# Optimization experiments

Hardware: AMD Instinct MI355X
Metric: run time of the kernel (lower is better)

Reference implementation:

```python
import jax, jax.numpy as jnp
import numpy as np

# MolFormer TestBert config (from checkpoint hyper_parameters)
B, T, D, H, L, F, V = 64, 250, 768, 12, 12, 32, 2362
DH = D // H  # head dim = 64
EPS = 1e-6   # fast_transformers LinearAttention eps


def _layernorm(x, g, b):
    m = x.mean(-1, keepdims=True)
    v = ((x - m) ** 2).mean(-1, keepdims=True)
    return (x - m) / jnp.sqrt(v + 1e-5) * g + b


def setup_inputs() -> dict:
    key = jax.random.key(0)
    ks = jax.random.split(key, 20)
    s = 0.02

    def n(k, shape, scale=s):
        return jax.random.normal(k, shape, dtype=jnp.float32) * scale

    mask = jax.random.randint(ks[1], (B, T), 0, 2).astype(bool)
    mask = mask.at[:, 0].set(True)  # keep CLS position valid
    return {
        "batch": jax.random.randint(ks[0], (B, T), 0, V),
        "mask": mask,
        "tok_emb": n(ks[2], (V, D)),
        "pos_emb": n(ks[3], (1, T, D)),
        "Wq": n(ks[4], (L, D, D)), "bq": jnp.zeros((L, D)),
        "Wk": n(ks[5], (L, D, D)), "bk": jnp.zeros((L, D)),
        "Wv": n(ks[6], (L, D, D)), "bv": jnp.zeros((L, D)),
        "Wo": n(ks[7], (L, D, D)), "bo": jnp.zeros((L, D)),
        # GeneralizedRandomFeatures random projection omega: [L, head_dim, n_feats]
        "omega": jax.random.normal(ks[8], (L, DH, F), dtype=jnp.float32),
        "ln1_g": jnp.ones((L, D)), "ln1_b": jnp.zeros((L, D)),
        "ln2_g": jnp.ones((L, D)), "ln2_b": jnp.zeros((L, D)),
        # feed_forward_dimensions == n_embd in the builder kwargs
        "W1": n(ks[9], (L, D, D)), "b1": jnp.zeros((L, D)),
        "W2": n(ks[10], (L, D, D)), "b2": jnp.zeros((L, D)),
    }


def reference(batch, mask, tok_emb, pos_emb, Wq, bq, Wk, bk, Wv, bv, Wo, bo,
              omega, ln1_g, ln1_b, ln2_g, ln2_b, W1, b1, W2, b2):
    Bc, Tc = batch.shape
    # LengthMask(mask.sum(-1)) -> prefix key mask
    lengths = mask.astype(jnp.int32).sum(-1)
    key_mask = (jnp.arange(Tc)[None, :] < lengths[:, None]).astype(jnp.float32)  # [B,T]

    x = tok_emb[batch] + pos_emb[:, :Tc, :]  # dropout = identity in eval
    attn_w = None
    for l in range(L):
        q = (x @ Wq[l] + bq[l]).reshape(Bc, Tc, H, DH)
        k = (x @ Wk[l] + bk[l]).reshape(Bc, Tc, H, DH)
        v = (x @ Wv[l] + bv[l]).reshape(Bc, Tc, H, DH)
        # GeneralizedRandomFeatures: phi(x) = relu(x @ omega)
        Qf = jax.nn.relu(jnp.einsum('bthd,df->bthf', q, omega[l]))
        Kf = jax.nn.relu(jnp.einsum('bshd,df->bshf', k, omega[l]))
        Kf = Kf * key_mask[:, :, None, None]
        # linear attention: out = phi(Q) (phi(K)^T V) / (phi(Q) . sum phi(K))
        KV = jnp.einsum('bshf,bshm->bhfm', Kf, v)
        Z = 1.0 / (jnp.einsum('bthf,bhf->bth', Qf, Kf.sum(axis=1)) + EPS)
        out = jnp.einsum('bthf,bhfm,bth->bthm', Qf, KV, Z)
        if l == L - 1:
            # 'linearwweights': the implied (normalized) attention matrix
            attn_w = jnp.einsum('bthf,bshf,bth->bhts', Qf, Kf, Z)
        out = out.reshape(Bc, Tc, D) @ Wo[l] + bo[l]
        # fast_transformers post-norm encoder layer
        x = _layernorm(x + out, ln1_g[l], ln1_b[l])
        y = jax.nn.gelu(x @ W1[l] + b1[l], approximate=False) @ W2[l] + b2[l]
        x = _layernorm(x + y, ln2_g[l], ln2_b[l])
    # mode == 'cls'
    return x[:, 0, :], attn_w
```

## Files before the change

kernel.cpp:

```cpp
#include <hip/hip_runtime.h>
#include <hip/hip_bf16.h>

typedef __hip_bfloat16 bf16;
typedef __attribute__((ext_vector_type(4))) float f32x4;
typedef __attribute__((ext_vector_type(8))) short bf16x8;
typedef __attribute__((ext_vector_type(4))) short short4v;

#define B_ 64
#define T_ 250
#define D_ 768
#define H_ 12
#define DH_ 64
#define F_ 32
#define L_ 12
#define BT_ (B_*T_)
#define NF_ (H_*F_)
#define QKVN_ (3*D_)
#define KVTN_ 80

static __device__ __forceinline__ float b2f(short s) {
    union { float f; unsigned u; } z; z.u = ((unsigned)(unsigned short)s) << 16; return z.f;
}
static __device__ __forceinline__ short f2bs(float f) {
    bf16 b = __float2bfloat16(f);
    return *(short*)&b;
}

__global__ void lengths_kernel(const unsigned char* __restrict__ mask, int* __restrict__ lengths) {
    __shared__ int not_i32, not_f32;
    const unsigned int* w = (const unsigned int*)mask;
    int tid = threadIdx.x;
    if (tid == 0) { not_i32 = 0; not_f32 = 0; }
    __syncthreads();
    int li = 0, lf = 0;
    for (int i = tid; i < 4000; i += 256) {
        unsigned int v = w[i];
        if (v > 1u) li = 1;
        if (v != 0u && v != 0x3F800000u) lf = 1;
    }
    if (li) not_i32 = 1;
    if (lf) not_f32 = 1;
    __syncthreads();
    int mode = (!not_i32) ? 0 : ((!not_f32) ? 1 : 2);
    if (tid < B_) {
        int cnt = 0;
        if (mode == 0) {
            const int* r = (const int*)mask + tid * T_;
            for (int t = 0; t < T_; ++t) cnt += (r[t] != 0);
        } else if (mode == 1) {
            const unsigned int* r = w + tid * T_;
            for (int t = 0; t < T_; ++t) cnt += (r[t] != 0);
        } else {
            const unsigned char* r = mask + tid * T_;
            for (int t = 0; t < T_; ++t) cnt += (r[t] != 0);
        }
        lengths[tid] = cnt;
    }
}

__global__ void embed_kernel(const int* __restrict__ batch, const float* __restrict__ tok,
                             const float* __restrict__ pos, float* __restrict__ x,
                             bf16* __restrict__ xb) {
    int bt = blockIdx.x;
    int t = bt % T_;
    int tok_id = batch[bt];
    const float* tr = tok + (size_t)tok_id * D_;
    const float* pr = pos + (size_t)t * D_;
    float* xr = x + (size_t)bt * D_;
    bf16* xbr = xb + (size_t)bt * D_;
    for (int d = threadIdx.x; d < D_; d += 256) {
        float v = tr[d] + pr[d];
        xr[d] = v;
        xbr[d] = __float2bfloat16(v);
    }
}

__global__ __launch_bounds__(256) void transpose_w_all(
    const float* __restrict__ Wq, const float* __restrict__ Wk, const float* __restrict__ Wv,
    const float* __restrict__ Wo, const float* __restrict__ W1, const float* __restrict__ W2,
    bf16* __restrict__ Wt)
{
    __shared__ float tile[32][33];
    int zz = blockIdx.z;
    int l = zz / 6, m = zz - l * 6;
    const float* src;
    switch (m) {
        case 0: src = Wq; break; case 1: src = Wk; break; case 2: src = Wv; break;
        case 3: src = Wo; break; case 4: src = W1; break; default: src = W2; break;
    }
    src += (size_t)l * D_ * D_;
    bf16* dst = Wt + (size_t)zz * D_ * D_;
    int k0 = blockIdx.y * 32, n0 = blockIdx.x * 32;
    int tx = threadIdx.x, ty = threadIdx.y;
#pragma unroll
    for (int i = 0; i < 4; ++i)
        tile[ty + i * 8][tx] = src[(size_t)(k0 + ty + i * 8) * D_ + n0 + tx];
    __syncthreads();
#pragma unroll
    for (int i = 0; i < 4; ++i)
        dst[(size_t)(n0 + ty + i * 8) * D_ + k0 + tx] = __float2bfloat16(tile[tx][ty + i * 8]);
}

__global__ void pack_bias(const float* __restrict__ bq, const float* __restrict__ bk,
                          const float* __restrict__ bv, float* __restrict__ qkvb) {
    int o = blockIdx.x * 256 + threadIdx.x;
    if (o >= L_ * QKVN_) return;
    int l = o / QKVN_, c = o - l * QKVN_;
    float v;
    if (c < D_) v = bq[l * D_ + c];
    else if (c < 2 * D_) v = bk[l * D_ + c - D_];
    else v = bv[l * D_ + c - 2 * D_];
    qkvb[o] = v;
}

#define GP_SLOT 20480
__global__ __launch_bounds__(512, 2) void gemm_pipe(
    const bf16* __restrict__ A, const bf16* __restrict__ Bt,
    const float* __restrict__ bias, bf16* __restrict__ C,
    int N, int lda, int ldc, int act, const int* __restrict__ lengths)
{
    __shared__ __attribute__((aligned(16))) short lds_s[3 * GP_SLOT];
    const int tid = threadIdx.x, lane = tid & 63, wave = tid >> 6;
    const int wm = wave >> 2, wn = wave & 3;
    const int rsel = lane & 15, kq = lane >> 4;

    const int gx = gridDim.x;
    const int nwg = gx * gridDim.y;
    int orig = blockIdx.y * gx + blockIdx.x;
    int q = nwg >> 3, r = nwg & 7;
    int xcd = orig & 7, idx = orig >> 3;
    int swz = (xcd < r) ? xcd * (q + 1) + idx : r * (q + 1) + (xcd - r) * q + idx;
    const int row0 = (swz / gx) * 128;
    const int col0 = (swz % gx) * 192;

    const short* gA[2];
    const short* gB[3];
#pragma unroll
    for (int i = 0; i < 2; ++i) {
        int seg = (i * 8 + wave) * 64 + lane;
        int rr = seg >> 3, kb = (seg & 7) ^ (rr & 7);
        gA[i] = (const short*)A + (size_t)(row0 + rr) * lda + kb * 8;
    }
#pragma unroll
    for (int i = 0; i < 3; ++i) {
        int seg = (i * 8 + wave) * 64 + lane;
        int rr = seg >> 3, kb = (seg & 7) ^ (rr & 7);
        gB[i] = (const short*)Bt + (size_t)(col0 + rr) * 768 + kb * 8;
    }

    f32x4 acc[4][3];
#pragma unroll
    for (int i = 0; i < 4; ++i)
#pragma unroll
        for (int j = 0; j < 3; ++j) acc[i][j] = (f32x4){0.f, 0.f, 0.f, 0.f};

    auto STAGE = [&](int kt, int slot) {
        short* base = lds_s + slot * GP_SLOT;
        int kcol = kt * 64;
#pragma unroll
        for (int i = 0; i < 2; ++i) {
            int segb = (i * 8 + wave) * 64;
            __builtin_amdgcn_global_load_lds(
                (const __attribute__((address_space(1))) unsigned int*)(gA[i] + kcol),
                (__attribute__((address_space(3))) unsigned int*)(base + segb * 8), 16, 0, 0);
        }
#pragma unroll
        for (int i = 0; i < 3; ++i) {
            int segb = (i * 8 + wave) * 64;
            __builtin_amdgcn_global_load_lds(
                (const __attribute__((address_space(1))) unsigned int*)(gB[i] + kcol),
                (__attribute__((address_space(3))) unsigned int*)(base + 8192 + segb * 8), 16, 0, 0);
        }
    };

    auto COMPUTE = [&](int slot) {
        const short* sA = lds_s + slot * GP_SLOT;
        const short* sB = sA + 8192;
        bf16x8 bfv[3][2];
#pragma unroll
        for (int n = 0; n < 3; ++n)
#pragma unroll
            for (int ks = 0; ks < 2; ++ks) {
                int rr = wn * 48 + n * 16 + rsel;
                int kb = ks * 4 + kq;
                bfv[n][ks] = *(const bf16x8*)(sB + rr * 64 + ((kb ^ (rr & 7)) << 3));
            }
#pragma unroll
        for (int mp = 0; mp < 2; ++mp) {
            bf16x8 af[2][2];
#pragma unroll
            for (int mi = 0; mi < 2; ++mi)
#pragma unroll
                for (int ks = 0; ks < 2; ++ks) {
                    int rr = wm * 64 + (mp * 2 + mi) * 16 + rsel;
                    int kb = ks * 4 + kq;
                    af[mi][ks] = *(const bf16x8*)(sA + rr * 64 + ((kb ^ (rr & 7)) << 3));
                }
            __builtin_amdgcn_s_setprio(1);
#pragma unroll
            for (int mi = 0; mi < 2; ++mi)
#pragma unroll
                for (int n = 0; n < 3; ++n)
#pragma unroll
                    for (int ks = 0; ks < 2; ++ks)
                        acc[mp * 2 + mi][n] = __builtin_amdgcn_mfma_f32_16x16x32_bf16(
                            af[mi][ks], bfv[n][ks], acc[mp * 2 + mi][n], 0, 0, 0);
            __builtin_amdgcn_s_setprio(0);
        }
    };

    STAGE(0, 0); STAGE(1, 1); STAGE(2, 2);
    asm volatile("s_waitcnt vmcnt(10)" ::: "memory");
    __builtin_amdgcn_s_barrier();

    int slot = 0;
    for (int kt = 0; kt < 12; ++kt) {
        COMPUTE(slot);
        if (kt < 11) {
            __builtin_amdgcn_s_barrier();
            if (kt <= 8) {
                STAGE(kt + 3, slot);
                asm volatile("s_waitcnt vmcnt(10)" ::: "memory");
            } else if (kt == 9) {
                asm volatile("s_waitcnt vmcnt(5)" ::: "memory");
            } else {
                asm volatile("s_waitcnt vmcnt(0)" ::: "memory");
            }
            __builtin_amdgcn_s_barrier();
        }
        slot = (slot == 2) ? 0 : slot + 1;
    }

    float bj[3];
#pragma unroll
    for (int n = 0; n < 3; ++n) {
        int col = col0 + wn * 48 + n * 16 + rsel;
        bj[n] = bias ? bias[col] : 0.f;
    }
#pragma unroll
    for (int m = 0; m < 4; ++m) {
#pragma unroll
        for (int rr = 0; rr < 4; ++rr) {
            int row = row0 + wm * 64 + m * 16 + (kq << 2) + rr;
            bool kill = false;
            if (act == 3) { int b = row / T_; int t = row - b * T_; kill = (t >= lengths[b]); }
            size_t base = (size_t)row * ldc + col0 + wn * 48 + rsel;
#pragma unroll
            for (int n = 0; n < 3; ++n) {
                float v = acc[m][n][rr] + bj[n];
                if (act == 1) v = 0.5f * v * (1.0f + erff(v * 0.70710678118654752f));
                else if (act >= 2) v = fmaxf(v, 0.f);
                if (kill) v = 0.f;
                C[base + n * 16] = __float2bfloat16(v);
            }
        }
    }
}

__global__ __launch_bounds__(256) void feat_kernel(
    const bf16* __restrict__ qkv, const float* __restrict__ om,
    bf16* __restrict__ Qf, bf16* __restrict__ Kf, const int* __restrict__ lengths)
{
    __shared__ __attribute__((aligned(16))) short omT[32 * 64];
    int z = blockIdx.z, h = blockIdx.y;
    int row0 = blockIdx.x * 128;
    int tid = threadIdx.x, lane = tid & 63, wave = tid >> 6;
    {
        int f = tid >> 3, k0 = (tid & 7) * 8;
#pragma unroll
        for (int j = 0; j < 8; ++j)
            omT[f * 64 + k0 + j] = f2bs(om[(size_t)(k0 + j) * F_ + f]);
    }
    __syncthreads();

    const short* A = (const short*)qkv + (size_t)z * D_ + h * DH_;
    int rsel = lane & 15, kof = (lane >> 4) << 3;

    bf16x8 af[2][2], bfr[2][2];
#pragma unroll
    for (int mi = 0; mi < 2; ++mi) {
        int row = row0 + wave * 32 + mi * 16 + rsel;
#pragma unroll
        for (int ks = 0; ks < 2; ++ks)
            af[mi][ks] = *(const bf16x8*)(A + (size_t)row * QKVN_ + ks * 32 + kof);
    }
#pragma unroll
    for (int ni = 0; ni < 2; ++ni)
#pragma unroll
        for (int ks = 0; ks < 2; ++ks)
            bfr[ni][ks] = *(const bf16x8*)(omT + (ni * 16 + rsel) * 64 + ks * 32 + kof);

    f32x4 acc[2][2];
#pragma unroll
    for (int i = 0; i < 2; ++i)
#pragma unroll
        for (int j = 0; j < 2; ++j) acc[i][j] = (f32x4){0.f, 0.f, 0.f, 0.f};
#pragma unroll
    for (int mi = 0; mi < 2; ++mi)
#pragma unroll
        for (int ni = 0; ni < 2; ++ni)
#pragma unroll
            for (int ks = 0; ks < 2; ++ks)
                acc[mi][ni] = __builtin_amdgcn_mfma_f32_16x16x32_bf16(af[mi][ks], bfr[ni][ks], acc[mi][ni], 0, 0, 0);

    bf16* out = z ? Kf : Qf;
#pragma unroll
    for (int mi = 0; mi < 2; ++mi) {
#pragma unroll
        for (int r = 0; r < 4; ++r) {
            int row = row0 + wave * 32 + mi * 16 + ((lane >> 4) << 2) + r;
            bool kill = false;
            if (z) { int b = row / T_; int t = row - b * T_; kill = (t >= lengths[b]); }
#pragma unroll
            for (int ni = 0; ni < 2; ++ni) {
                float v = fmaxf(acc[mi][ni][r], 0.f);
                if (kill) v = 0.f;
                out[(size_t)row * NF_ + h * F_ + ni * 16 + rsel] = __float2bfloat16(v);
            }
        }
    }
}

__global__ __launch_bounds__(256) void kvsum_kernel(
    const bf16* __restrict__ Kf, const bf16* __restrict__ v, int ldv,
    bf16* __restrict__ KVt)
{
    __shared__ short KfS[64][36];
    __shared__ short vS[64][68];
    int h = blockIdx.x, b = blockIdx.y;
    int tid = threadIdx.x, lane = tid & 63, wv = tid >> 6;
    int lr = tid >> 2, cp = tid & 3;

    const short* Kg = (const short*)Kf + (size_t)(b * T_) * NF_ + h * F_;
    const short* Vg = (const short*)v + (size_t)(b * T_) * ldv + h * DH_;

    f32x4 acc[2];
    acc[0] = (f32x4){0.f, 0.f, 0.f, 0.f};
    acc[1] = (f32x4){0.f, 0.f, 0.f, 0.f};
    float ksacc = 0.f;

    for (int s0 = 0; s0 < T_; s0 += 64) {
        __syncthreads();
        int s = s0 + lr;
        if (s < T_) {
            bf16x8 k8 = *(const bf16x8*)(Kg + (size_t)s * NF_ + cp * 8);
            *(short4v*)&KfS[lr][cp * 8]     = *((const short4v*)&k8);
            *(short4v*)&KfS[lr][cp * 8 + 4] = *((const short4v*)&k8 + 1);
            bf16x8 v8a = *(const bf16x8*)(Vg + (size_t)s * ldv + cp * 16);
            bf16x8 v8b = *(const bf16x8*)(Vg + (size_t)s * ldv + cp * 16 + 8);
            *(short4v*)&vS[lr][cp * 16]      = *((const short4v*)&v8a);
            *(short4v*)&vS[lr][cp * 16 + 4]  = *((const short4v*)&v8a + 1);
            *(short4v*)&vS[lr][cp * 16 + 8]  = *((const short4v*)&v8b);
            *(short4v*)&vS[lr][cp * 16 + 12] = *((const short4v*)&v8b + 1);
        } else {
            short4v zz = (short4v){0, 0, 0, 0};
            *(short4v*)&KfS[lr][cp * 8]     = zz;
            *(short4v*)&KfS[lr][cp * 8 + 4] = zz;
            *(short4v*)&vS[lr][cp * 16]      = zz;
            *(short4v*)&vS[lr][cp * 16 + 4]  = zz;
            *(short4v*)&vS[lr][cp * 16 + 8]  = zz;
            *(short4v*)&vS[lr][cp * 16 + 12] = zz;
        }
        __syncthreads();
        if (tid < 32) {
            float p0 = 0.f, p1 = 0.f;
            for (int ss = 0; ss < 64; ss += 2) {
                p0 += b2f(KfS[ss][tid]);
                p1 += b2f(KfS[ss + 1][tid]);
            }
            ksacc += p0 + p1;
        }
        bf16x8 af0[2], af1[2], bfr[2];
#pragma unroll
        for (int ks = 0; ks < 2; ++ks) {
            int sb = ks * 32 + ((lane >> 4) << 3);
#pragma unroll
            for (int j = 0; j < 8; ++j) {
                ((short*)&af0[ks])[j] = KfS[sb + j][lane & 15];
                ((short*)&af1[ks])[j] = KfS[sb + j][16 + (lane & 15)];
                ((short*)&bfr[ks])[j] = vS[sb + j][wv * 16 + (lane & 15)];
            }
        }
#pragma unroll
        for (int ks = 0; ks < 2; ++ks) {
            acc[0] = __builtin_amdgcn_mfma_f32_16x16x32_bf16(af0[ks], bfr[ks], acc[0], 0, 0, 0);
            acc[1] = __builtin_amdgcn_mfma_f32_16x16x32_bf16(af1[ks], bfr[ks], acc[1], 0, 0, 0);
        }
    }

    bf16* dst = KVt + (size_t)(b * H_ + h) * KVTN_ * F_;
    int m = wv * 16 + (lane & 15);
#pragma unroll
    for (int mi = 0; mi < 2; ++mi) {
#pragma unroll
        for (int r = 0; r < 4; ++r) {
            int f = mi * 16 + ((lane >> 4) << 2) + r;
            dst[(size_t)m * F_ + f] = __float2bfloat16(acc[mi][r]);
        }
    }
    if (tid < 32) dst[(size_t)64 * F_ + tid] = __float2bfloat16(ksacc);
    if (tid < 240) {
        ((short*)dst)[65 * F_ + tid * 2]     = 0;
        ((short*)dst)[65 * F_ + tid * 2 + 1] = 0;
    }
}

__global__ __launch_bounds__(256) void attn_mfma(
    const bf16* __restrict__ Qf, const bf16* __restrict__ KVt,
    float* __restrict__ Z, bf16* __restrict__ out, int ldo)
{
    int h = blockIdx.x, b = blockIdx.y;
    int tid = threadIdx.x, lane = tid & 63, wv = tid >> 6;
    int t0 = wv * 64;
    int rsel = lane & 15, kof = (lane >> 4) << 3;

    const short* Qg = (const short*)Qf + h * F_;
    const short* Bg = (const short*)KVt + (size_t)(b * H_ + h) * KVTN_ * F_;

    bf16x8 af[4], bfr[5];
#pragma unroll
    for (int mi = 0; mi < 4; ++mi) {
        int t = t0 + mi * 16 + rsel;
        if (t > T_ - 1) t = T_ - 1;
        af[mi] = *(const bf16x8*)(Qg + (size_t)(b * T_ + t) * NF_ + kof);
    }
#pragma unroll
    for (int ni = 0; ni < 5; ++ni)
        bfr[ni] = *(const bf16x8*)(Bg + (size_t)(ni * 16 + rsel) * F_ + kof);

    f32x4 acc[4][5];
#pragma unroll
    for (int i = 0; i < 4; ++i)
#pragma unroll
        for (int j = 0; j < 5; ++j) acc[i][j] = (f32x4){0.f, 0.f, 0.f, 0.f};
#pragma unroll
    for (int mi = 0; mi < 4; ++mi)
#pragma unroll
        for (int ni = 0; ni < 5; ++ni)
            acc[mi][ni] = __builtin_amdgcn_mfma_f32_16x16x32_bf16(af[mi], bfr[ni], acc[mi][ni], 0, 0, 0);

#pragma unroll
    for (int mi = 0; mi < 4; ++mi) {
#pragma unroll
        for (int r = 0; r < 4; ++r) {
            int t = t0 + mi * 16 + ((lane >> 4) << 2) + r;
            float zden = __shfl(acc[mi][4][r], lane & 48, 64);
            float z = 1.0f / (zden + 1e-6f);
            if (t < T_) {
                if (rsel == 0) Z[(size_t)(b * T_ + t) * H_ + h] = z;
                size_t base = (size_t)(b * T_ + t) * ldo + h * DH_ + rsel;
#pragma unroll
                for (int ni = 0; ni < 4; ++ni)
                    out[base + ni * 16] = __float2bfloat16(acc[mi][ni][r] * z);
            }
        }
    }
}

__global__ __launch_bounds__(256) void attnw_kernel(const bf16* __restrict__ Qf,
                                                    const bf16* __restrict__ Kf,
                                                    const float* __restrict__ Z,
                                                    float* __restrict__ out) {
    int tt = blockIdx.x;
    int bh = blockIdx.y;
    int b = bh / H_, h = bh - b * H_;
    int tid = threadIdx.x;
    int lane = tid & 63, w = tid >> 6;
    int t0 = tt * 64, s0 = w * 64;
    int kof = (lane >> 4) * 8;

    const short* Qs = (const short*)Qf;
    const short* Ks = (const short*)Kf;

    bf16x8 af[4], bfr[4];
#pragma unroll
    for (int mi = 0; mi < 4; ++mi) {
        int t = t0 + mi * 16 + (lane & 15);
        if (t > T_ - 1) t = T_ - 1;
        af[mi] = *(const bf16x8*)(Qs + ((size_t)(b * T_ + t) * H_ + h) * F_ + kof);
    }
#pragma unroll
    for (int ni = 0; ni < 4; ++ni) {
        int s = s0 + ni * 16 + (lane & 15);
        if (s > T_ - 1) s = T_ - 1;
        bfr[ni] = *(const bf16x8*)(Ks + ((size_t)(b * T_ + s) * H_ + h) * F_ + kof);
    }

    f32x4 acc[4][4];
#pragma unroll
    for (int i = 0; i < 4; ++i)
#pragma unroll
        for (int j = 0; j < 4; ++j) acc[i][j] = (f32x4){0.f, 0.f, 0.f, 0.f};
#pragma unroll
    for (int mi = 0; mi < 4; ++mi)
#pragma unroll
        for (int ni = 0; ni < 4; ++ni)
            acc[mi][ni] = __builtin_amdgcn_mfma_f32_16x16x32_bf16(af[mi], bfr[ni], acc[mi][ni], 0, 0, 0);

#pragma unroll
    for (int mi = 0; mi < 4; ++mi) {
#pragma unroll
        for (int r = 0; r < 4; ++r) {
            int t = t0 + mi * 16 + (lane >> 4) * 4 + r;
            if (t >= T_) continue;
            float z = Z[(size_t)(b * T_ + t) * H_ + h];
            size_t base = ((size_t)bh * T_ + t) * T_;
#pragma unroll
            for (int ni = 0; ni < 4; ++ni) {
                int s = s0 + ni * 16 + (lane & 15);
                if (s < T_) out[base + s] = acc[mi][ni][r] * z;
            }
        }
    }
}

__global__ __launch_bounds__(256) void ln_kernel(float* __restrict__ x, const bf16* __restrict__ res,
                                                 int ldr,
                                                 const float* __restrict__ g, const float* __restrict__ bb,
                                                 bf16* __restrict__ xb) {
    int bt = blockIdx.x, tid = threadIdx.x;
    float* xr = x + (size_t)bt * D_;
    const bf16* rr = res + (size_t)bt * ldr;
    float v[3]; float s = 0.f, ss = 0.f;
#pragma unroll
    for (int i = 0; i < 3; ++i) {
        int idx = tid + i * 256;
        float t = xr[idx] + __bfloat162float(rr[idx]);
        v[i] = t; s += t; ss += t * t;
    }
#pragma unroll
    for (int o = 1; o < 64; o <<= 1) { s += __shfl_xor(s, o, 64); ss += __shfl_xor(ss, o, 64); }
    __shared__ float red[4][2];
    int wave = tid >> 6, lane = tid & 63;
    if (lane == 0) { red[wave][0] = s; red[wave][1] = ss; }
    __syncthreads();
    s = red[0][0] + red[1][0] + red[2][0] + red[3][0];
    ss = red[0][1] + red[1][1] + red[2][1] + red[3][1];
    float mean = s * (1.f / D_);
    float var = ss * (1.f / D_) - mean * mean;
    float rstd = rsqrtf(var + 1e-5f);
    bf16* xbr = xb + (size_t)bt * D_;
#pragma unroll
    for (int i = 0; i < 3; ++i) {
        int idx = tid + i * 256;
        float o = (v[i] - mean) * rstd * g[idx] + bb[idx];
        xr[idx] = o;
        xbr[idx] = __float2bfloat16(o);
    }
}

__global__ void cls_kernel(const float* __restrict__ x, float* __restrict__ out) {
    int o = blockIdx.x * 256 + threadIdx.x;
    if (o >= B_ * D_) return;
    int b = o / D_, d = o % D_;
    out[o] = x[(size_t)(b * T_) * D_ + d];
}

extern "C" void kernel_launch(void* const* d_in, const int* in_sizes, int n_in,
                              void* d_out, int out_size, void* d_ws, size_t ws_size,
                              hipStream_t stream) {
    const int*   batch = (const int*)d_in[0];
    const unsigned char* mask = (const unsigned char*)d_in[1];
    const float* tok  = (const float*)d_in[2];
    const float* pos  = (const float*)d_in[3];
    const float* Wq   = (const float*)d_in[4];
    const float* bq   = (const float*)d_in[5];
    const float* Wk   = (const float*)d_in[6];
    const float* bk   = (const float*)d_in[7];
    const float* Wv   = (const float*)d_in[8];
    const float* bv   = (const float*)d_in[9];
    const float* Wo   = (const float*)d_in[10];
    const float* bo   = (const float*)d_in[11];
    const float* omega= (const float*)d_in[12];
    const float* ln1g = (const float*)d_in[13];
    const float* ln1b = (const float*)d_in[14];
    const float* ln2g = (const float*)d_in[15];
    const float* ln2b = (const float*)d_in[16];
    const float* W1   = (const float*)d_in[17];
    const float* b1   = (const float*)d_in[18];
    const float* W2   = (const float*)d_in[19];
    const float* b2   = (const float*)d_in[20];

    float* out_cls  = (float*)d_out;
    float* out_attn = (float*)d_out + B_ * D_;

    char* wsb = (char*)d_ws;
    float* x   = (float*)wsb; wsb += (size_t)BT_ * D_ * 4;
    bf16* xb   = (bf16*)wsb;  wsb += (size_t)BT_ * D_ * 2;
    bf16* qkv  = (bf16*)wsb;  wsb += (size_t)BT_ * QKVN_ * 2;
    bf16* Qf   = (bf16*)wsb;  wsb += (size_t)BT_ * NF_ * 2;
    bf16* Kf   = (bf16*)wsb;  wsb += (size_t)BT_ * NF_ * 2;
    bf16* KVt  = (bf16*)wsb;  wsb += (size_t)B_ * H_ * KVTN_ * F_ * 2;
    float* Z   = (float*)wsb; wsb += (size_t)BT_ * H_ * 4;
    bf16* Wt   = (bf16*)wsb;  wsb += (size_t)L_ * 6 * D_ * D_ * 2;
    float* qkvb= (float*)wsb; wsb += (size_t)L_ * QKVN_ * 4;
    int* lengths = (int*)wsb; wsb += 256;

    lengths_kernel<<<1, 256, 0, stream>>>(mask, lengths);
    embed_kernel<<<BT_, 256, 0, stream>>>(batch, tok, pos, x, xb);
    pack_bias<<<(L_ * QKVN_ + 255) / 256, 256, 0, stream>>>(bq, bk, bv, qkvb);
    transpose_w_all<<<dim3(24, 24, 72), dim3(32, 8), 0, stream>>>(Wq, Wk, Wv, Wo, W1, W2, Wt);

    dim3 qkv_g(QKVN_ / 192, BT_ / 128);
    dim3 dxd_g(D_ / 192, BT_ / 128);
    dim3 feat_g(BT_ / 128, H_, 2);
    dim3 kv_g(H_, B_);
    const size_t WS = (size_t)D_ * D_;

    for (int l = 0; l < L_; ++l) {
        const bf16* Wtl = Wt + (size_t)l * 6 * WS;

        gemm_pipe<<<qkv_g, 512, 0, stream>>>(xb, Wtl, qkvb + l * QKVN_, qkv,
                                             QKVN_, D_, QKVN_, 0, lengths);

        feat_kernel<<<feat_g, 256, 0, stream>>>(qkv, omega + (size_t)l * DH_ * F_,
                                                Qf, Kf, lengths);

        kvsum_kernel<<<kv_g, 256, 0, stream>>>(Kf, qkv + 2 * D_, QKVN_, KVt);

        attn_mfma<<<kv_g, 256, 0, stream>>>(Qf, KVt, Z, qkv, QKVN_);

        if (l == L_ - 1)
            attnw_kernel<<<dim3(4, B_ * H_), 256, 0, stream>>>(Qf, Kf, Z, out_attn);

        gemm_pipe<<<dxd_g, 512, 0, stream>>>(qkv, Wtl + 3 * WS, bo + l * D_, qkv + D_,
                                             D_, QKVN_, QKVN_, 0, lengths);
        ln_kernel<<<BT_, 256, 0, stream>>>(x, qkv + D_, QKVN_, ln1g + l * D_, ln1b + l * D_, xb);

        gemm_pipe<<<dxd_g, 512, 0, stream>>>(xb, Wtl + 4 * WS, b1 + l * D_, qkv + 2 * D_,
                                             D_, D_, QKVN_, 1, lengths);
        gemm_pipe<<<dxd_g, 512, 0, stream>>>(qkv + 2 * D_, Wtl + 5 * WS, b2 + l * D_, qkv,
                                             D_, QKVN_, QKVN_, 0, lengths);
        ln_kernel<<<BT_, 256, 0, stream>>>(x, qkv, QKVN_, ln2g + l * D_, ln2b + l * D_, xb);
    }

    cls_kernel<<<(B_ * D_ + 255) / 256, 256, 0, stream>>>(x, out_cls);
}
```

Measured before the change: 3.565 ms.

## Enlarge GEMM tile to 256x192 with double-buffered LDS and padded rows

Doubles the GEMM M-tile from 128 to 256 rows, so each workgroup runs 8x3 MFMA accumulator tiles per wave. LDS staging drops from three stages to two, and the loads are restructured into simpler per-wave row segments. The token dimension is padded to 16128 rows so the grid divides evenly, and the xb and qkv buffers are enlarged to match. This aims to raise operand reuse and arithmetic intensity per loaded byte. The costs are a larger LDS footprint, which likely allows only one workgroup per CU, shallower prefetch, wasted work on padded rows, and possible out-of-bounds writes into any unpadded output buffers.

```diff
diff --git a/kernel.cpp b/kernel.cpp
--- a/kernel.cpp
+++ b/kernel.cpp
@@ -14,6 +14,7 @@
 #define F_ 32
 #define L_ 12
 #define BT_ (B_*T_)
+#define BT_P 16128
 #define NF_ (H_*F_)
 #define QKVN_ (3*D_)
 #define KVTN_ 80
@@ -113,13 +114,13 @@
     qkvb[o] = v;
 }
 
-#define GP_SLOT 20480
+#define GP_SLOT 28672
 __global__ __launch_bounds__(512, 2) void gemm_pipe(
     const bf16* __restrict__ A, const bf16* __restrict__ Bt,
     const float* __restrict__ bias, bf16* __restrict__ C,
     int N, int lda, int ldc, int act, const int* __restrict__ lengths)
 {
-    __shared__ __attribute__((aligned(16))) short lds_s[3 * GP_SLOT];
+    __shared__ __attribute__((aligned(16))) short lds_s[2 * GP_SLOT];
     const int tid = threadIdx.x, lane = tid & 63, wave = tid >> 6;
     const int wm = wave >> 2, wn = wave & 3;
     const int rsel = lane & 15, kq = lane >> 4;
@@ -130,105 +131,84 @@
     int q = nwg >> 3, r = nwg & 7;
     int xcd = orig & 7, idx = orig >> 3;
     int swz = (xcd < r) ? xcd * (q + 1) + idx : r * (q + 1) + (xcd - r) * q + idx;
-    const int row0 = (swz / gx) * 128;
+    const int row0 = (swz / gx) * 256;
     const int col0 = (swz % gx) * 192;
 
-    const short* gA[2];
-    const short* gB[3];
-#pragma unroll
-    for (int i = 0; i < 2; ++i) {
-        int seg = (i * 8 + wave) * 64 + lane;
-        int rr = seg >> 3, kb = (seg & 7) ^ (rr & 7);
-        gA[i] = (const short*)A + (size_t)(row0 + rr) * lda + kb * 8;
-    }
-#pragma unroll
-    for (int i = 0; i < 3; ++i) {
-        int seg = (i * 8 + wave) * 64 + lane;
-        int rr = seg >> 3, kb = (seg & 7) ^ (rr & 7);
-        gB[i] = (const short*)Bt + (size_t)(col0 + rr) * 768 + kb * 8;
-    }
-
-    f32x4 acc[4][3];
-#pragma unroll
-    for (int i = 0; i < 4; ++i)
+    const int srow = wave * 8 + (lane >> 3);
+    const int sblk = (lane & 7) ^ ((lane >> 3) & 7);
+    const short* gA = (const short*)A + (size_t)(row0 + srow) * lda + sblk * 8;
+    const short* gB = (const short*)Bt + (size_t)(col0 + srow) * 768 + sblk * 8;
+    const int ldest = wave * 512;
+
+    f32x4 acc[8][3];
+#pragma unroll
+    for (int i = 0; i < 8; ++i)
 #pragma unroll
         for (int j = 0; j < 3; ++j) acc[i][j] = (f32x4){0.f, 0.f, 0.f, 0.f};
 
     auto STAGE = [&](int kt, int slot) {
         short* base = lds_s + slot * GP_SLOT;
-        int kcol = kt * 64;
-#pragma unroll
-        for (int i = 0; i < 2; ++i) {
-            int segb = (i * 8 + wave) * 64;
+        int kc = kt * 64;
+#pragma unroll
+        for (int j = 0; j < 4; ++j)
             __builtin_amdgcn_global_load_lds(
-                (const __attribute__((address_space(1))) unsigned int*)(gA[i] + kcol),
-                (__attribute__((address_space(3))) unsigned int*)(base + segb * 8), 16, 0, 0);
-        }
-#pragma unroll
-        for (int i = 0; i < 3; ++i) {
-            int segb = (i * 8 + wave) * 64;
+                (const __attribute__((address_space(1))) unsigned int*)(gA + (size_t)(j * 64) * lda + kc),
+                (__attribute__((address_space(3))) unsigned int*)(base + j * 4096 + ldest), 16, 0, 0);
+#pragma unroll
+        for (int j = 0; j < 3; ++j)
             __builtin_amdgcn_global_load_lds(
-                (const __attribute__((address_space(1))) unsigned int*)(gB[i] + kcol),
-                (__attribute__((address_space(3))) unsigned int*)(base + 8192 + segb * 8), 16, 0, 0);
-        }
+                (const __attribute__((address_space(1))) unsigned int*)(gB + (size_t)(j * 64) * 768 + kc),
+                (__attribute__((address_space(3))) unsigned int*)(base + 16384 + j * 4096 + ldest), 16, 0, 0);
     };
 
     auto COMPUTE = [&](int slot) {
         const short* sA = lds_s + slot * GP_SLOT;
-        const short* sB = sA + 8192;
-        bf16x8 bfv[3][2];
-#pragma unroll
-        for (int n = 0; n < 3; ++n)
-#pragma unroll
-            for (int ks = 0; ks < 2; ++ks) {
-                int rr = wn * 48 + n * 16 + rsel;
-                int kb = ks * 4 + kq;
-                bfv[n][ks] = *(const bf16x8*)(sB + rr * 64 + ((kb ^ (rr & 7)) << 3));
-            }
-#pragma unroll
-        for (int mp = 0; mp < 2; ++mp) {
-            bf16x8 af[2][2];
-#pragma unroll
-            for (int mi = 0; mi < 2; ++mi)
-#pragma unroll
-                for (int ks = 0; ks < 2; ++ks) {
-                    int rr = wm * 64 + (mp * 2 + mi) * 16 + rsel;
-                    int kb = ks * 4 + kq;
-                    af[mi][ks] = *(const bf16x8*)(sA + rr * 64 + ((kb ^ (rr & 7)) << 3));
+        const short* sB = sA + 16384;
+#pragma unroll
+        for (int ks = 0; ks < 2; ++ks) {
+            int kb = ks * 4 + kq;
+            bf16x8 bv[3];
+#pragma unroll
+            for (int n = 0; n < 3; ++n) {
+                int rowb = wn * 48 + n * 16 + rsel;
+                bv[n] = *(const bf16x8*)(sB + rowb * 64 + ((kb ^ (rowb & 7)) << 3));
+            }
+#pragma unroll
+            for (int mh = 0; mh < 2; ++mh) {
+                bf16x8 av[4];
+#pragma unroll
+                for (int m2 = 0; m2 < 4; ++m2) {
+                    int rowa = wm * 128 + (mh * 4 + m2) * 16 + rsel;
+                    av[m2] = *(const bf16x8*)(sA + rowa * 64 + ((kb ^ (rowa & 7)) << 3));
                 }
-            __builtin_amdgcn_s_setprio(1);
-#pragma unroll
-            for (int mi = 0; mi < 2; ++mi)
-#pragma unroll
-                for (int n = 0; n < 3; ++n)
-#pragma unroll
-                    for (int ks = 0; ks < 2; ++ks)
-                        acc[mp * 2 + mi][n] = __builtin_amdgcn_mfma_f32_16x16x32_bf16(
-                            af[mi][ks], bfv[n][ks], acc[mp * 2 + mi][n], 0, 0, 0);
-            __builtin_amdgcn_s_setprio(0);
+                __builtin_amdgcn_s_setprio(1);
+#pragma unroll
+                for (int m2 = 0; m2 < 4; ++m2)
+#pragma unroll
+                    for (int n = 0; n < 3; ++n)
+                        acc[mh * 4 + m2][n] = __builtin_amdgcn_mfma_f32_16x16x32_bf16(
+                            av[m2], bv[n], acc[mh * 4 + m2][n], 0, 0, 0);
+                __builtin_amdgcn_s_setprio(0);
+            }
         }
     };
 
-    STAGE(0, 0); STAGE(1, 1); STAGE(2, 2);
-    asm volatile("s_waitcnt vmcnt(10)" ::: "memory");
+    STAGE(0, 0); STAGE(1, 1);
+    asm volatile("s_waitcnt vmcnt(7)" ::: "memory");
     __builtin_amdgcn_s_barrier();
 
-    int slot = 0;
-    for (int kt = 0; kt < 12; ++kt) {
-        COMPUTE(slot);
-        if (kt < 11) {
+    for (int t = 0; t < 12; ++t) {
+        COMPUTE(t & 1);
+        if (t < 11) {
             __builtin_amdgcn_s_barrier();
-            if (kt <= 8) {
-                STAGE(kt + 3, slot);
-                asm volatile("s_waitcnt vmcnt(10)" ::: "memory");
-            } else if (kt == 9) {
-                asm volatile("s_waitcnt vmcnt(5)" ::: "memory");
+            if (t < 10) {
+                STAGE(t + 2, t & 1);
+                asm volatile("s_waitcnt vmcnt(7)" ::: "memory");
             } else {
                 asm volatile("s_waitcnt vmcnt(0)" ::: "memory");
             }
             __builtin_amdgcn_s_barrier();
         }
-        slot = (slot == 2) ? 0 : slot + 1;
     }
 
     float bj[3];
@@ -238,16 +218,16 @@
         bj[n] = bias ? bias[col] : 0.f;
     }
 #pragma unroll
-    for (int m = 0; m < 4; ++m) {
+    for (int mi = 0; mi < 8; ++mi) {
 #pragma unroll
         for (int rr = 0; rr < 4; ++rr) {
-            int row = row0 + wm * 64 + m * 16 + (kq << 2) + rr;
+            int row = row0 + wm * 128 + mi * 16 + (kq << 2) + rr;
             bool kill = false;
-            if (act == 3) { int b = row / T_; int t = row - b * T_; kill = (t >= lengths[b]); }
+            if (act == 3) { int b = row / T_; int t = row - b * T_; kill = (t >= lengths[b & 63]); }
             size_t base = (size_t)row * ldc + col0 + wn * 48 + rsel;
 #pragma unroll
             for (int n = 0; n < 3; ++n) {
-                float v = acc[m][n][rr] + bj[n];
+                float v = acc[mi][n][rr] + bj[n];
                 if (act == 1) v = 0.5f * v * (1.0f + erff(v * 0.70710678118654752f));
                 else if (act >= 2) v = fmaxf(v, 0.f);
                 if (kill) v = 0.f;
@@ -586,8 +566,8 @@
 
     char* wsb = (char*)d_ws;
     float* x   = (float*)wsb; wsb += (size_t)BT_ * D_ * 4;
-    bf16* xb   = (bf16*)wsb;  wsb += (size_t)BT_ * D_ * 2;
-    bf16* qkv  = (bf16*)wsb;  wsb += (size_t)BT_ * QKVN_ * 2;
+    bf16* xb   = (bf16*)wsb;  wsb += (size_t)BT_P * D_ * 2;
+    bf16* qkv  = (bf16*)wsb;  wsb += (size_t)BT_P * QKVN_ * 2;
     bf16* Qf   = (bf16*)wsb;  wsb += (size_t)BT_ * NF_ * 2;
     bf16* Kf   = (bf16*)wsb;  wsb += (size_t)BT_ * NF_ * 2;
     bf16* KVt  = (bf16*)wsb;  wsb += (size_t)B_ * H_ * KVTN_ * F_ * 2;
@@ -601,8 +581,8 @@
     pack_bias<<<(L_ * QKVN_ + 255) / 256, 256, 0, stream>>>(bq, bk, bv, qkvb);
     transpose_w_all<<<dim3(24, 24, 72), dim3(32, 8), 0, stream>>>(Wq, Wk, Wv, Wo, W1, W2, Wt);
 
-    dim3 qkv_g(QKVN_ / 192, BT_ / 128);
-    dim3 dxd_g(D_ / 192, BT_ / 128);
+    dim3 qkv_g(QKVN_ / 192, BT_P / 256);
+    dim3 dxd_g(D_ / 192, BT_P / 256);
     dim3 feat_g(BT_ / 128, H_, 2);
     dim3 kv_g(H_, B_);
     const size_t WS = (size_t)D_ * D_;
```

Result: faster. 3.353 ms (-5.9%).
